# Kernel tuning notes

Measured on AMD Instinct MI355X. Metric: run time of the kernel, lower is better.

The kernel has to match this reference:

```python
import jax, jax.numpy as jnp
import numpy as np

N_NODES = 100000
N_EDGES = 1600000
NIN = 128
NHID = 128
N_GRAPHS = 1024


def _gcn_conv(x, src, dst, norm, W, b, n_nodes):
    """PyG-style GCNConv: linear (no bias) -> normalized scatter-add -> + bias."""
    xw = x @ W                                   # [N, out]
    msg = xw[src] * norm[:, None]                # gather + edge-normalize, [E', out]
    out = jax.ops.segment_sum(msg, dst, num_segments=n_nodes)
    return out + b


def _gcn_norm(edge_index, n_nodes):
    """Add self-loops and compute symmetric deg^{-1/2} normalization per edge."""
    loops = jnp.arange(n_nodes, dtype=edge_index.dtype)
    src = jnp.concatenate([edge_index[0], loops])
    dst = jnp.concatenate([edge_index[1], loops])
    deg = jax.ops.segment_sum(jnp.ones_like(dst, dtype=jnp.float32), dst,
                              num_segments=n_nodes)
    deg_isqrt = jnp.where(deg > 0, jax.lax.rsqrt(jnp.maximum(deg, 1.0)), 0.0)
    norm = deg_isqrt[src] * deg_isqrt[dst]
    return src, dst, norm


def setup_inputs() -> dict:
    key = jax.random.key(0)
    ks = jax.random.split(key, 8)
    x = jax.random.normal(ks[0], (N_NODES, NIN), dtype=jnp.float32)
    edge_index = jax.random.randint(ks[1], (2, N_EDGES), 0, N_NODES, dtype=jnp.int64)
    batch = jnp.sort(jax.random.randint(ks[2], (N_NODES,), 0, N_GRAPHS, dtype=jnp.int64))
    s_in = 1.0 / np.sqrt(NIN)
    s_h = 1.0 / np.sqrt(NHID)
    return {
        "x": x,
        "edge_index": edge_index,
        "batch": batch,
        "W1": jax.random.normal(ks[3], (NIN, NHID), dtype=jnp.float32) * s_in,
        "b1": jnp.zeros((NHID,), dtype=jnp.float32),
        "W2": jax.random.normal(ks[4], (NHID, NHID), dtype=jnp.float32) * s_h,
        "b2": jnp.zeros((NHID,), dtype=jnp.float32),
        "W3": jax.random.normal(ks[5], (NHID, NHID), dtype=jnp.float32) * s_h,
        "b3": jnp.zeros((NHID,), dtype=jnp.float32),
        "Wfc": jax.random.normal(ks[6], (NHID, 1), dtype=jnp.float32) * s_h,
        "bfc": jnp.zeros((1,), dtype=jnp.float32),
    }


def reference(x, edge_index, batch, W1, b1, W2, b2, W3, b3, Wfc, bfc):
    n_nodes = x.shape[0]
    src, dst, norm = _gcn_norm(edge_index, n_nodes)
    h = jax.nn.relu(_gcn_conv(x, src, dst, norm, W1, b1, n_nodes))
    h = jax.nn.relu(_gcn_conv(h, src, dst, norm, W2, b2, n_nodes))
    h = jax.nn.relu(_gcn_conv(h, src, dst, norm, W3, b3, n_nodes))
    # global mean pool over graphs in the batch
    sums = jax.ops.segment_sum(h, batch, num_segments=N_GRAPHS)      # [G, NHID]
    cnts = jax.ops.segment_sum(jnp.ones((n_nodes,), dtype=h.dtype), batch,
                               num_segments=N_GRAPHS)
    pooled = sums / jnp.maximum(cnts, 1.0)[:, None]
    return pooled @ Wfc + bfc                                        # [G, 1]
```

## Files before the change

### kernel.cpp

```cpp
#include <hip/hip_runtime.h>

#define N_NODES   100000
#define N_EDGES   1600000
#define NFEAT     128
#define N_GRAPHS  1024

#define BSHIFT  8
#define BNODES  256
#define NBUCK   391
#define BCAP    4608
#define SC_EDGES 8192
#define SC_BLOCKS 196

typedef unsigned int uint32;
typedef unsigned short ushort;
typedef __attribute__((ext_vector_type(8))) short short8;
typedef __attribute__((ext_vector_type(4))) float f32x4;

__device__ inline ushort f2b(float f) {
    uint32 x = __float_as_uint(f);
    uint32 r = x + 0x7fffu + ((x >> 16) & 1u);
    return (ushort)(r >> 16);
}
__device__ inline float blo(uint32 u) { return __uint_as_float(u << 16); }
__device__ inline float bhi(uint32 u) { return __uint_as_float(u & 0xffff0000u); }

__global__ __launch_bounds__(256) void k_scatter(const int* __restrict__ src, const int* __restrict__ dst,
                                                 int* __restrict__ cur, uint32* __restrict__ bbuf) {
    __shared__ int hist[NBUCK];
    __shared__ int lofs[NBUCK];
    __shared__ int lcur[NBUCK];
    __shared__ int gbase[NBUCK];
    __shared__ int wsum[4];
    __shared__ uint32 sortedP[SC_EDGES];
    __shared__ ushort sortedB[SC_EDGES];
    int t = threadIdx.x;
    int e0 = blockIdx.x * SC_EDGES;
    int total = N_EDGES - e0; if (total > SC_EDGES) total = SC_EDGES; if (total < 0) total = 0;

    for (int i = t; i < NBUCK; i += 256) hist[i] = 0;
    __syncthreads();
    for (int i = t; i < total; i += 256)
        atomicAdd(&hist[dst[e0 + i] >> BSHIFT], 1);
    __syncthreads();
    {
        int b0 = 2 * t, b1 = 2 * t + 1;
        int h0 = (b0 < NBUCK) ? hist[b0] : 0;
        int h1 = (b1 < NBUCK) ? hist[b1] : 0;
        int ts = h0 + h1;
        int lane = t & 63, w = t >> 6;
        int inc = ts;
        #pragma unroll
        for (int d = 1; d < 64; d <<= 1) {
            int u = __shfl_up(inc, d, 64);
            if (lane >= d) inc += u;
        }
        if (lane == 63) wsum[w] = inc;
        __syncthreads();
        int wpre = 0;
        for (int i = 0; i < w; ++i) wpre += wsum[i];
        int run = wpre + inc - ts;
        if (b0 < NBUCK) {
            lofs[b0] = run; lcur[b0] = run;
            if (h0) gbase[b0] = atomicAdd(&cur[b0], h0);
        }
        if (b1 < NBUCK) {
            lofs[b1] = run + h0; lcur[b1] = run + h0;
            if (h1) gbase[b1] = atomicAdd(&cur[b1], h1);
        }
    }
    __syncthreads();
    for (int i = t; i < total; i += 256) {
        int s = src[e0 + i], d = dst[e0 + i];
        int b = d >> BSHIFT;
        int p = atomicAdd(&lcur[b], 1);
        sortedP[p] = ((uint32)(d & (BNODES - 1)) << 17) | (uint32)s;
        sortedB[p] = (ushort)b;
    }
    __syncthreads();
    for (int i = t; i < total; i += 256) {
        int b = sortedB[i];
        int addr = gbase[b] + (i - lofs[b]);
        if (addr < BCAP)
            bbuf[(size_t)b * BCAP + addr] = sortedP[i];
    }
}

__global__ __launch_bounds__(256) void k_bucketscan(const int* __restrict__ cur, int* __restrict__ bucketBase,
                                                    int* __restrict__ offsets) {
    __shared__ int wsum[4];
    int t = threadIdx.x;
    int b0 = 2 * t, b1 = 2 * t + 1;
    int h0 = 0, h1 = 0;
    if (b0 < NBUCK) { h0 = cur[b0]; if (h0 > BCAP) h0 = BCAP; }
    if (b1 < NBUCK) { h1 = cur[b1]; if (h1 > BCAP) h1 = BCAP; }
    int ts = h0 + h1;
    int lane = t & 63, w = t >> 6;
    int inc = ts;
    #pragma unroll
    for (int d = 1; d < 64; d <<= 1) {
        int u = __shfl_up(inc, d, 64);
        if (lane >= d) inc += u;
    }
    if (lane == 63) wsum[w] = inc;
    __syncthreads();
    int wpre = 0;
    for (int i = 0; i < w; ++i) wpre += wsum[i];
    int run = wpre + inc - ts;
    if (b0 < NBUCK) bucketBase[b0] = run;
    if (b1 < NBUCK) bucketBase[b1] = run + h0;
    if (t == 255) offsets[N_NODES] = run + ts;
}

__global__ __launch_bounds__(256) void k_build(const uint32* __restrict__ bbuf, const int* __restrict__ cur,
                                               const int* __restrict__ bucketBase, int* __restrict__ col,
                                               int* __restrict__ offsets, float* __restrict__ dinv) {
    int b = blockIdx.x;
    __shared__ int hist[BNODES], lcur[BNODES];
    __shared__ int wsum[4];
    __shared__ int sorted[BCAP];
    int t = threadIdx.x;
    int cnt = cur[b]; if (cnt > BCAP) cnt = BCAP;
    const uint32* reg = bbuf + (size_t)b * BCAP;
    hist[t] = 0;
    __syncthreads();
    for (int i = t; i < cnt; i += 256) atomicAdd(&hist[reg[i] >> 17], 1);
    __syncthreads();
    {
        int c = hist[t];
        int lane = t & 63, w = t >> 6;
        int inc = c;
        #pragma unroll
        for (int d = 1; d < 64; d <<= 1) {
            int u = __shfl_up(inc, d, 64);
            if (lane >= d) inc += u;
        }
        if (lane == 63) wsum[w] = inc;
        __syncthreads();
        int wpre = 0;
        for (int i = 0; i < w; ++i) wpre += wsum[i];
        int excl = wpre + inc - c;
        lcur[t] = excl;
        int node = (b << BSHIFT) + t;
        if (node < N_NODES) {
            offsets[node] = bucketBase[b] + excl;
            dinv[node] = rsqrtf((float)(c + 1));
        }
    }
    __syncthreads();
    for (int i = t; i < cnt; i += 256) {
        uint32 p = reg[i];
        int lp = atomicAdd(&lcur[p >> 17], 1);
        sorted[lp] = (int)(p & 0x1FFFF);
    }
    __syncthreads();
    int base = bucketBase[b];
    for (int i = t; i < cnt; i += 256) col[base + i] = sorted[i];
}

__global__ __launch_bounds__(256) void k_castw(const float* __restrict__ W1, const float* __restrict__ W2,
                                               const float* __restrict__ W3, ushort* __restrict__ WT) {
    int i = blockIdx.x * blockDim.x + threadIdx.x;
    if (i >= 3 * NFEAT * NFEAT) return;
    int l = i >> 14;
    int j = i & 16383;
    int n = j >> 7;
    int k = j & 127;
    const float* W = (l == 0) ? W1 : (l == 1) ? W2 : W3;
    WT[i] = f2b(W[k * NFEAT + n]);
}

#define WT_STRIDE 136
#define GEMM_EPILOGUE \
    __syncthreads(); \
    { \
        ushort* sC = sWT; \
        int colBase = lane & 15; \
        _Pragma("unroll") \
        for (int r = 0; r < 4; ++r) { \
            int lr = wave * 16 + kg * 4 + r; \
            _Pragma("unroll") \
            for (int nt = 0; nt < 8; ++nt) \
                sC[lr * NFEAT + nt * 16 + colBase] = f2b(acc[nt][r]); \
        } \
    } \
    __syncthreads(); \
    { \
        int rowBase = blockIdx.x * 128; \
        const float4* sC4 = (const float4*)sWT; \
        for (int i = t; i < 2048; i += 512) { \
            int row = i >> 4; \
            int gr = rowBase + row; \
            if (gr < M) ((float4*)(C + (size_t)gr * NFEAT))[i & 15] = sC4[i]; \
        } \
    }

__global__ __launch_bounds__(512) void k_gemm(const ushort* __restrict__ A,
                                              const ushort* __restrict__ WTl,
                                              ushort* __restrict__ C, int M) {
    __shared__ ushort sWT[NFEAT * WT_STRIDE];
    int t = threadIdx.x;
    for (int i = t; i < NFEAT * 16; i += 512) {
        int n = i >> 4, c = i & 15;
        *(float4*)(sWT + n * WT_STRIDE + c * 8) = ((const float4*)WTl)[i];
    }
    int wave = t >> 6, lane = t & 63;
    int m0 = blockIdx.x * 128 + wave * 16;
    int mRow = m0 + (lane & 15);
    if (mRow >= M) mRow = M - 1;
    int kg = lane >> 4;
    const short8* Ap = (const short8*)(A + (size_t)mRow * NFEAT + kg * 8);
    short8 a0 = Ap[0];
    short8 a1 = Ap[4];
    short8 a2 = Ap[8];
    short8 a3 = Ap[12];
    __syncthreads();

    f32x4 acc[8];
    #pragma unroll
    for (int nt = 0; nt < 8; ++nt) acc[nt] = (f32x4){0.f, 0.f, 0.f, 0.f};

    #pragma unroll
    for (int nt = 0; nt < 8; ++nt) {
        int n = nt * 16 + (lane & 15);
        const short8* Bp = (const short8*)(sWT + n * WT_STRIDE + kg * 8);
        short8 b0 = Bp[0];
        short8 b1 = Bp[4];
        short8 b2 = Bp[8];
        short8 b3 = Bp[12];
        acc[nt] = __builtin_amdgcn_mfma_f32_16x16x32_bf16(a0, b0, acc[nt], 0, 0, 0);
        acc[nt] = __builtin_amdgcn_mfma_f32_16x16x32_bf16(a1, b1, acc[nt], 0, 0, 0);
        acc[nt] = __builtin_amdgcn_mfma_f32_16x16x32_bf16(a2, b2, acc[nt], 0, 0, 0);
        acc[nt] = __builtin_amdgcn_mfma_f32_16x16x32_bf16(a3, b3, acc[nt], 0, 0, 0);
    }
    GEMM_EPILOGUE
}

__device__ inline short8 cvt8(const float* p) {
    float4 v0 = ((const float4*)p)[0];
    float4 v1 = ((const float4*)p)[1];
    short8 r;
    r[0] = (short)f2b(v0.x); r[1] = (short)f2b(v0.y);
    r[2] = (short)f2b(v0.z); r[3] = (short)f2b(v0.w);
    r[4] = (short)f2b(v1.x); r[5] = (short)f2b(v1.y);
    r[6] = (short)f2b(v1.z); r[7] = (short)f2b(v1.w);
    return r;
}

__global__ __launch_bounds__(512) void k_gemm_x(const float* __restrict__ A,
                                                const ushort* __restrict__ WTl,
                                                ushort* __restrict__ C, int M) {
    __shared__ ushort sWT[NFEAT * WT_STRIDE];
    int t = threadIdx.x;
    for (int i = t; i < NFEAT * 16; i += 512) {
        int n = i >> 4, c = i & 15;
        *(float4*)(sWT + n * WT_STRIDE + c * 8) = ((const float4*)WTl)[i];
    }
    int wave = t >> 6, lane = t & 63;
    int m0 = blockIdx.x * 128 + wave * 16;
    int mRow = m0 + (lane & 15);
    if (mRow >= M) mRow = M - 1;
    int kg = lane >> 4;
    const float* Ap = A + (size_t)mRow * NFEAT + kg * 8;
    short8 a0 = cvt8(Ap);
    short8 a1 = cvt8(Ap + 32);
    short8 a2 = cvt8(Ap + 64);
    short8 a3 = cvt8(Ap + 96);
    __syncthreads();

    f32x4 acc[8];
    #pragma unroll
    for (int nt = 0; nt < 8; ++nt) acc[nt] = (f32x4){0.f, 0.f, 0.f, 0.f};

    #pragma unroll
    for (int nt = 0; nt < 8; ++nt) {
        int n = nt * 16 + (lane & 15);
        const short8* Bp = (const short8*)(sWT + n * WT_STRIDE + kg * 8);
        short8 b0 = Bp[0];
        short8 b1 = Bp[4];
        short8 b2 = Bp[8];
        short8 b3 = Bp[12];
        acc[nt] = __builtin_amdgcn_mfma_f32_16x16x32_bf16(a0, b0, acc[nt], 0, 0, 0);
        acc[nt] = __builtin_amdgcn_mfma_f32_16x16x32_bf16(a1, b1, acc[nt], 0, 0, 0);
        acc[nt] = __builtin_amdgcn_mfma_f32_16x16x32_bf16(a2, b2, acc[nt], 0, 0, 0);
        acc[nt] = __builtin_amdgcn_mfma_f32_16x16x32_bf16(a3, b3, acc[nt], 0, 0, 0);
    }
    GEMM_EPILOGUE
}

#define AGG_BODY4 \
    float dn = dinv[n]; \
    int half = lane >> 4; \
    int fl = lane & 15; \
    const uint4* XW4 = (const uint4*)XWu; \
    uint4 sv = XW4[(size_t)n * 16 + fl]; \
    float ws = (half == 0) ? dn * dn : 0.f; \
    float a0 = ws * blo(sv.x), a1 = ws * bhi(sv.x); \
    float a2 = ws * blo(sv.y), a3 = ws * bhi(sv.y); \
    float a4 = ws * blo(sv.z), a5 = ws * bhi(sv.z); \
    float a6 = ws * blo(sv.w), a7 = ws * bhi(sv.w); \
    int e0 = off[n], e1 = off[n + 1]; \
    for (int base = e0; base < e1; base += 64) { \
        int len = e1 - base; if (len > 64) len = 64; \
        int cm = (lane < len) ? col[base + lane] : 0; \
        float wm = (lane < len) ? dn * dinv[cm] : 0.f; \
        int j = 0; \
        for (; j + 16 <= len; j += 16) { \
            uint4 u[4]; float w[4]; \
            _Pragma("unroll") \
            for (int p = 0; p < 4; ++p) { \
                int idx = j + 4 * p + half; \
                int cc = __shfl(cm, idx, 64); \
                w[p] = __shfl(wm, idx, 64); \
                u[p] = XW4[(size_t)cc * 16 + fl]; \
            } \
            _Pragma("unroll") \
            for (int p = 0; p < 4; ++p) { \
                a0 = fmaf(w[p], blo(u[p].x), a0); a1 = fmaf(w[p], bhi(u[p].x), a1); \
                a2 = fmaf(w[p], blo(u[p].y), a2); a3 = fmaf(w[p], bhi(u[p].y), a3); \
                a4 = fmaf(w[p], blo(u[p].z), a4); a5 = fmaf(w[p], bhi(u[p].z), a5); \
                a6 = fmaf(w[p], blo(u[p].w), a6); a7 = fmaf(w[p], bhi(u[p].w), a7); \
            } \
        } \
        for (; j < len; j += 4) { \
            int rem = len - j; \
            int idx = j + ((half < rem) ? half : 0); \
            int cc = __shfl(cm, idx, 64); \
            float ww = __shfl(wm, idx, 64); \
            if (half >= rem) ww = 0.f; \
            uint4 u = XW4[(size_t)cc * 16 + fl]; \
            a0 = fmaf(ww, blo(u.x), a0); a1 = fmaf(ww, bhi(u.x), a1); \
            a2 = fmaf(ww, blo(u.y), a2); a3 = fmaf(ww, bhi(u.y), a3); \
            a4 = fmaf(ww, blo(u.z), a4); a5 = fmaf(ww, bhi(u.z), a5); \
            a6 = fmaf(ww, blo(u.w), a6); a7 = fmaf(ww, bhi(u.w), a7); \
        } \
    } \
    a0 += __shfl_xor(a0, 32, 64); a0 += __shfl_xor(a0, 16, 64); \
    a1 += __shfl_xor(a1, 32, 64); a1 += __shfl_xor(a1, 16, 64); \
    a2 += __shfl_xor(a2, 32, 64); a2 += __shfl_xor(a2, 16, 64); \
    a3 += __shfl_xor(a3, 32, 64); a3 += __shfl_xor(a3, 16, 64); \
    a4 += __shfl_xor(a4, 32, 64); a4 += __shfl_xor(a4, 16, 64); \
    a5 += __shfl_xor(a5, 32, 64); a5 += __shfl_xor(a5, 16, 64); \
    a6 += __shfl_xor(a6, 32, 64); a6 += __shfl_xor(a6, 16, 64); \
    a7 += __shfl_xor(a7, 32, 64); a7 += __shfl_xor(a7, 16, 64);

__global__ __launch_bounds__(256) void k_agg(const uint32* __restrict__ XWu, const int* __restrict__ col,
                                             const int* __restrict__ off, const float* __restrict__ dinv,
                                             const float* __restrict__ bias, uint32* __restrict__ Hu) {
    int wid = (blockIdx.x * blockDim.x + threadIdx.x) >> 6;
    int lane = threadIdx.x & 63;
    if (wid >= N_NODES) return;
    int n = wid;
    AGG_BODY4
    if (half == 0) {
        float4 bb0 = ((const float4*)bias)[2 * fl];
        float4 bb1 = ((const float4*)bias)[2 * fl + 1];
        float r0 = fmaxf(a0 + bb0.x, 0.f), r1 = fmaxf(a1 + bb0.y, 0.f);
        float r2 = fmaxf(a2 + bb0.z, 0.f), r3 = fmaxf(a3 + bb0.w, 0.f);
        float r4 = fmaxf(a4 + bb1.x, 0.f), r5 = fmaxf(a5 + bb1.y, 0.f);
        float r6 = fmaxf(a6 + bb1.z, 0.f), r7 = fmaxf(a7 + bb1.w, 0.f);
        uint4 o;
        o.x = (uint32)f2b(r0) | ((uint32)f2b(r1) << 16);
        o.y = (uint32)f2b(r2) | ((uint32)f2b(r3) << 16);
        o.z = (uint32)f2b(r4) | ((uint32)f2b(r5) << 16);
        o.w = (uint32)f2b(r6) | ((uint32)f2b(r7) << 16);
        ((uint4*)Hu)[(size_t)n * 16 + fl] = o;
    }
}

__global__ __launch_bounds__(256) void k_agg_fc(const uint32* __restrict__ XWu, const int* __restrict__ col,
                                                const int* __restrict__ off, const float* __restrict__ dinv,
                                                const float* __restrict__ bias, const float* __restrict__ Wfc,
                                                float* __restrict__ nodeS) {
    int wid = (blockIdx.x * blockDim.x + threadIdx.x) >> 6;
    int lane = threadIdx.x & 63;
    if (wid >= N_NODES) return;
    int n = wid;
    AGG_BODY4
    float4 bb0 = ((const float4*)bias)[2 * fl];
    float4 bb1 = ((const float4*)bias)[2 * fl + 1];
    float4 wf0 = ((const float4*)Wfc)[2 * fl];
    float4 wf1 = ((const float4*)Wfc)[2 * fl + 1];
    float s = fmaxf(a0 + bb0.x, 0.f) * wf0.x + fmaxf(a1 + bb0.y, 0.f) * wf0.y
            + fmaxf(a2 + bb0.z, 0.f) * wf0.z + fmaxf(a3 + bb0.w, 0.f) * wf0.w
            + fmaxf(a4 + bb1.x, 0.f) * wf1.x + fmaxf(a5 + bb1.y, 0.f) * wf1.y
            + fmaxf(a6 + bb1.z, 0.f) * wf1.z + fmaxf(a7 + bb1.w, 0.f) * wf1.w;
    s += __shfl_xor(s, 8, 64);
    s += __shfl_xor(s, 4, 64);
    s += __shfl_xor(s, 2, 64);
    s += __shfl_xor(s, 1, 64);
    if (lane == 0) nodeS[n] = s;
}

__device__ inline int lower_bound_dev(const int* a, int n, int key) {
    int lo = 0, hi = n;
    while (lo < hi) {
        int mid = (lo + hi) >> 1;
        if (a[mid] < key) lo = mid + 1; else hi = mid;
    }
    return lo;
}

__global__ __launch_bounds__(256) void k_pool(const float* __restrict__ nodeS, const int* __restrict__ batch,
                                              const float* __restrict__ bfc, float* __restrict__ out) {
    int g = blockIdx.x;
    int t = threadIdx.x;
    int lo = lower_bound_dev(batch, N_NODES, g);
    int hi = lower_bound_dev(batch, N_NODES, g + 1);
    float s = 0.f;
    for (int i = lo + t; i < hi; i += 256) s += nodeS[i];
    for (int d = 32; d > 0; d >>= 1) s += __shfl_down(s, d, 64);
    __shared__ float ws[4];
    int lane = t & 63, w = t >> 6;
    if (lane == 0) ws[w] = s;
    __syncthreads();
    if (t == 0) {
        float tot = ws[0] + ws[1] + ws[2] + ws[3];
        float cnt = (float)(hi - lo);
        out[g] = tot / fmaxf(cnt, 1.0f) + bfc[0];
    }
}

extern "C" void kernel_launch(void* const* d_in, const int* in_sizes, int n_in,
                              void* d_out, int out_size, void* d_ws, size_t ws_size,
                              hipStream_t stream) {
    const float* x    = (const float*)d_in[0];
    const int*   ei   = (const int*)d_in[1];
    const int*   batch= (const int*)d_in[2];
    const float* W1   = (const float*)d_in[3];
    const float* b1   = (const float*)d_in[4];
    const float* W2   = (const float*)d_in[5];
    const float* b2   = (const float*)d_in[6];
    const float* W3   = (const float*)d_in[7];
    const float* b3   = (const float*)d_in[8];
    const float* Wfc  = (const float*)d_in[9];
    const float* bfc  = (const float*)d_in[10];
    float* out = (float*)d_out;

    const int* src = ei;
    const int* dst = ei + N_EDGES;

    char* p = (char*)d_ws;
    auto carve = [&](size_t bytes) { void* r = (void*)p; p += (bytes + 255) & ~(size_t)255; return r; };
    int*    cur       = (int*)   carve(sizeof(int) * NBUCK);
    uint32* bbuf      = (uint32*)carve(sizeof(uint32) * (size_t)NBUCK * BCAP);
    int*    bucketBase= (int*)   carve(sizeof(int) * (NBUCK + 1));
    float*  dinv      = (float*) carve(sizeof(float) * N_NODES);
    int*    offsets   = (int*)   carve(sizeof(int) * (N_NODES + 1));
    int*    col       = (int*)   carve(sizeof(int) * N_EDGES);
    ushort* XW        = (ushort*)carve(sizeof(short) * (size_t)N_NODES * NFEAT);
    ushort* H         = (ushort*)carve(sizeof(short) * (size_t)N_NODES * NFEAT);
    ushort* WT        = (ushort*)carve(sizeof(short) * 3 * NFEAT * NFEAT);
    float*  nodeS     = (float*) carve(sizeof(float) * N_NODES);

    const int waveNodeBlocks = (N_NODES * 64 + 255) / 256;
    const int gemmBlocks = (N_NODES + 127) / 128;

    hipMemsetAsync(cur, 0, sizeof(int) * NBUCK, stream);
    k_scatter<<<SC_BLOCKS, 256, 0, stream>>>(src, dst, cur, bbuf);
    k_bucketscan<<<1, 256, 0, stream>>>(cur, bucketBase, offsets);
    k_build<<<NBUCK, 256, 0, stream>>>(bbuf, cur, bucketBase, col, offsets, dinv);

    k_castw<<<(3 * NFEAT * NFEAT + 255) / 256, 256, 0, stream>>>(W1, W2, W3, WT);

    k_gemm_x<<<gemmBlocks, 512, 0, stream>>>(x, WT, XW, N_NODES);
    k_agg<<<waveNodeBlocks, 256, 0, stream>>>((const uint32*)XW, col, offsets, dinv, b1, (uint32*)H);
    k_gemm<<<gemmBlocks, 512, 0, stream>>>(H, WT + NFEAT * NFEAT, XW, N_NODES);
    k_agg<<<waveNodeBlocks, 256, 0, stream>>>((const uint32*)XW, col, offsets, dinv, b2, (uint32*)H);
    k_gemm<<<gemmBlocks, 512, 0, stream>>>(H, WT + 2 * NFEAT * NFEAT, XW, N_NODES);
    k_agg_fc<<<waveNodeBlocks, 256, 0, stream>>>((const uint32*)XW, col, offsets, dinv, b3, Wfc, nodeS);

    k_pool<<<N_GRAPHS, 256, 0, stream>>>(nodeS, batch, bfc, out);
}
```

Measured before the change: 392.4 us.

## Fold bucket scan into build and weight cast into GEMMs; persistent multi-tile GEMM

Removes the standalone single-block bucket-scan kernel: each build block now computes its own bucket base by reducing the clamped bucket counts, and the last block writes the total edge count. Removes the weight-cast kernel: each GEMM block converts and transposes the fp32 weights into bf16 shared memory itself. The GEMM is restructured so each block keeps its B fragments in registers and loops over four 64-row tiles, with waves split across column halves. This cuts two launches and their serial dependencies, at the cost of redundant weight conversion and bucket reduction per block and more register pressure.

New measurement: 419.0 us. 1.07x slower.

```diff
diff --git a/kernel.cpp b/kernel.cpp
--- a/kernel.cpp
+++ b/kernel.cpp
@@ -86,44 +86,42 @@
     }
 }
 
-__global__ __launch_bounds__(256) void k_bucketscan(const int* __restrict__ cur, int* __restrict__ bucketBase,
-                                                    int* __restrict__ offsets) {
-    __shared__ int wsum[4];
-    int t = threadIdx.x;
-    int b0 = 2 * t, b1 = 2 * t + 1;
-    int h0 = 0, h1 = 0;
-    if (b0 < NBUCK) { h0 = cur[b0]; if (h0 > BCAP) h0 = BCAP; }
-    if (b1 < NBUCK) { h1 = cur[b1]; if (h1 > BCAP) h1 = BCAP; }
-    int ts = h0 + h1;
-    int lane = t & 63, w = t >> 6;
-    int inc = ts;
-    #pragma unroll
-    for (int d = 1; d < 64; d <<= 1) {
-        int u = __shfl_up(inc, d, 64);
-        if (lane >= d) inc += u;
-    }
-    if (lane == 63) wsum[w] = inc;
-    __syncthreads();
-    int wpre = 0;
-    for (int i = 0; i < w; ++i) wpre += wsum[i];
-    int run = wpre + inc - ts;
-    if (b0 < NBUCK) bucketBase[b0] = run;
-    if (b1 < NBUCK) bucketBase[b1] = run + h0;
-    if (t == 255) offsets[N_NODES] = run + ts;
-}
-
 __global__ __launch_bounds__(256) void k_build(const uint32* __restrict__ bbuf, const int* __restrict__ cur,
-                                               const int* __restrict__ bucketBase, int* __restrict__ col,
-                                               int* __restrict__ offsets, float* __restrict__ dinv) {
+                                               int* __restrict__ col, int* __restrict__ offsets,
+                                               float* __restrict__ dinv) {
     int b = blockIdx.x;
     __shared__ int hist[BNODES], lcur[BNODES];
-    __shared__ int wsum[4];
+    __shared__ int wsum[4], wtot[4];
     __shared__ int sorted[BCAP];
+    __shared__ int sBase, sTotal;
     int t = threadIdx.x;
+    {
+        int pre = 0, tot = 0;
+        #pragma unroll
+        for (int q = 0; q < 2; ++q) {
+            int i = 2 * t + q;
+            if (i < NBUCK) {
+                int v = cur[i]; if (v > BCAP) v = BCAP;
+                tot += v;
+                if (i < b) pre += v;
+            }
+        }
+        int lane = t & 63, w = t >> 6;
+        #pragma unroll
+        for (int d = 32; d > 0; d >>= 1) { pre += __shfl_down(pre, d, 64); tot += __shfl_down(tot, d, 64); }
+        if (lane == 0) { wsum[w] = pre; wtot[w] = tot; }
+        __syncthreads();
+        if (t == 0) {
+            sBase = wsum[0] + wsum[1] + wsum[2] + wsum[3];
+            sTotal = wtot[0] + wtot[1] + wtot[2] + wtot[3];
+        }
+        hist[t] = 0;
+    }
+    __syncthreads();
+    int base = sBase;
+    if (b == NBUCK - 1 && t == 0) offsets[N_NODES] = sTotal;
     int cnt = cur[b]; if (cnt > BCAP) cnt = BCAP;
     const uint32* reg = bbuf + (size_t)b * BCAP;
-    hist[t] = 0;
-    __syncthreads();
     for (int i = t; i < cnt; i += 256) atomicAdd(&hist[reg[i] >> 17], 1);
     __syncthreads();
     {
@@ -143,7 +141,7 @@
         lcur[t] = excl;
         int node = (b << BSHIFT) + t;
         if (node < N_NODES) {
-            offsets[node] = bucketBase[b] + excl;
+            offsets[node] = base + excl;
             dinv[node] = rsqrtf((float)(c + 1));
         }
     }
@@ -154,86 +152,81 @@
         sorted[lp] = (int)(p & 0x1FFFF);
     }
     __syncthreads();
-    int base = bucketBase[b];
     for (int i = t; i < cnt; i += 256) col[base + i] = sorted[i];
 }
 
-__global__ __launch_bounds__(256) void k_castw(const float* __restrict__ W1, const float* __restrict__ W2,
-                                               const float* __restrict__ W3, ushort* __restrict__ WT) {
-    int i = blockIdx.x * blockDim.x + threadIdx.x;
-    if (i >= 3 * NFEAT * NFEAT) return;
-    int l = i >> 14;
-    int j = i & 16383;
-    int n = j >> 7;
-    int k = j & 127;
-    const float* W = (l == 0) ? W1 : (l == 1) ? W2 : W3;
-    WT[i] = f2b(W[k * NFEAT + n]);
-}
-
 #define WT_STRIDE 136
-#define GEMM_EPILOGUE \
+#define GEMM_TILES 4
+
+#define GEMM_PROLOGUE(AFRAG_LOADS) \
+    __shared__ ushort sWT[NFEAT * WT_STRIDE];    \
+    __shared__ ushort sC[64 * NFEAT];            \
+    int t = threadIdx.x; \
+     \
+    for (int i = t; i < NFEAT * 32; i += 512) { \
+        int k = i >> 5, n0 = (i & 31) * 4; \
+        float4 v = ((const float4*)Wl)[i]; \
+        sWT[(n0 + 0) * WT_STRIDE + k] = f2b(v.x); \
+        sWT[(n0 + 1) * WT_STRIDE + k] = f2b(v.y); \
+        sWT[(n0 + 2) * WT_STRIDE + k] = f2b(v.z); \
+        sWT[(n0 + 3) * WT_STRIDE + k] = f2b(v.w); \
+    } \
+    int wave = t >> 6, lane = t & 63; \
+    int ch = wave & 1;           \
+    int rg = wave >> 1;          \
+    int kg = lane >> 4; \
+    int colBase = lane & 15; \
     __syncthreads(); \
-    { \
-        ushort* sC = sWT; \
-        int colBase = lane & 15; \
+     \
+    short8 bfr[4][4]; \
+    _Pragma("unroll") \
+    for (int nt = 0; nt < 4; ++nt) { \
+        int n = ch * 64 + nt * 16 + colBase; \
+        const short8* Bp = (const short8*)(sWT + n * WT_STRIDE + kg * 8); \
+        bfr[nt][0] = Bp[0]; bfr[nt][1] = Bp[4]; bfr[nt][2] = Bp[8]; bfr[nt][3] = Bp[12]; \
+    } \
+    int blockBase = blockIdx.x * (64 * GEMM_TILES); \
+    for (int tile = 0; tile < GEMM_TILES; ++tile) { \
+        int tb = blockBase + tile * 64; \
+        int m0 = tb + rg * 16; \
+        int mRow = m0 + colBase; \
+        if (mRow >= M) mRow = M - 1; \
+        short8 a0, a1, a2, a3; \
+        AFRAG_LOADS \
+        f32x4 acc[4]; \
+        _Pragma("unroll") \
+        for (int nt = 0; nt < 4; ++nt) acc[nt] = (f32x4){0.f, 0.f, 0.f, 0.f}; \
+        _Pragma("unroll") \
+        for (int nt = 0; nt < 4; ++nt) { \
+            acc[nt] = __builtin_amdgcn_mfma_f32_16x16x32_bf16(a0, bfr[nt][0], acc[nt], 0, 0, 0); \
+            acc[nt] = __builtin_amdgcn_mfma_f32_16x16x32_bf16(a1, bfr[nt][1], acc[nt], 0, 0, 0); \
+            acc[nt] = __builtin_amdgcn_mfma_f32_16x16x32_bf16(a2, bfr[nt][2], acc[nt], 0, 0, 0); \
+            acc[nt] = __builtin_amdgcn_mfma_f32_16x16x32_bf16(a3, bfr[nt][3], acc[nt], 0, 0, 0); \
+        } \
+        __syncthreads();    \
         _Pragma("unroll") \
         for (int r = 0; r < 4; ++r) { \
-            int lr = wave * 16 + kg * 4 + r; \
+            int rowLocal = rg * 16 + kg * 4 + r; \
             _Pragma("unroll") \
-            for (int nt = 0; nt < 8; ++nt) \
-                sC[lr * NFEAT + nt * 16 + colBase] = f2b(acc[nt][r]); \
+            for (int nt = 0; nt < 4; ++nt) \
+                sC[rowLocal * NFEAT + ch * 64 + nt * 16 + colBase] = f2b(acc[nt][r]); \
         } \
-    } \
-    __syncthreads(); \
-    { \
-        int rowBase = blockIdx.x * 128; \
-        const float4* sC4 = (const float4*)sWT; \
-        for (int i = t; i < 2048; i += 512) { \
+        __syncthreads(); \
+        const float4* sC4 = (const float4*)sC; \
+        for (int i = t; i < 1024; i += 512) { \
             int row = i >> 4; \
-            int gr = rowBase + row; \
+            int gr = tb + row; \
             if (gr < M) ((float4*)(C + (size_t)gr * NFEAT))[i & 15] = sC4[i]; \
         } \
     }
 
 __global__ __launch_bounds__(512) void k_gemm(const ushort* __restrict__ A,
-                                              const ushort* __restrict__ WTl,
+                                              const float* __restrict__ Wl,
                                               ushort* __restrict__ C, int M) {
-    __shared__ ushort sWT[NFEAT * WT_STRIDE];
-    int t = threadIdx.x;
-    for (int i = t; i < NFEAT * 16; i += 512) {
-        int n = i >> 4, c = i & 15;
-        *(float4*)(sWT + n * WT_STRIDE + c * 8) = ((const float4*)WTl)[i];
-    }
-    int wave = t >> 6, lane = t & 63;
-    int m0 = blockIdx.x * 128 + wave * 16;
-    int mRow = m0 + (lane & 15);
-    if (mRow >= M) mRow = M - 1;
-    int kg = lane >> 4;
-    const short8* Ap = (const short8*)(A + (size_t)mRow * NFEAT + kg * 8);
-    short8 a0 = Ap[0];
-    short8 a1 = Ap[4];
-    short8 a2 = Ap[8];
-    short8 a3 = Ap[12];
-    __syncthreads();
-
-    f32x4 acc[8];
-    #pragma unroll
-    for (int nt = 0; nt < 8; ++nt) acc[nt] = (f32x4){0.f, 0.f, 0.f, 0.f};
-
-    #pragma unroll
-    for (int nt = 0; nt < 8; ++nt) {
-        int n = nt * 16 + (lane & 15);
-        const short8* Bp = (const short8*)(sWT + n * WT_STRIDE + kg * 8);
-        short8 b0 = Bp[0];
-        short8 b1 = Bp[4];
-        short8 b2 = Bp[8];
-        short8 b3 = Bp[12];
-        acc[nt] = __builtin_amdgcn_mfma_f32_16x16x32_bf16(a0, b0, acc[nt], 0, 0, 0);
-        acc[nt] = __builtin_amdgcn_mfma_f32_16x16x32_bf16(a1, b1, acc[nt], 0, 0, 0);
-        acc[nt] = __builtin_amdgcn_mfma_f32_16x16x32_bf16(a2, b2, acc[nt], 0, 0, 0);
-        acc[nt] = __builtin_amdgcn_mfma_f32_16x16x32_bf16(a3, b3, acc[nt], 0, 0, 0);
-    }
-    GEMM_EPILOGUE
+    GEMM_PROLOGUE({
+        const short8* Ap = (const short8*)(A + (size_t)mRow * NFEAT + kg * 8);
+        a0 = Ap[0]; a1 = Ap[4]; a2 = Ap[8]; a3 = Ap[12];
+    })
 }
 
 __device__ inline short8 cvt8(const float* p) {
@@ -248,44 +241,12 @@
 }
 
 __global__ __launch_bounds__(512) void k_gemm_x(const float* __restrict__ A,
-                                                const ushort* __restrict__ WTl,
+                                                const float* __restrict__ Wl,
                                                 ushort* __restrict__ C, int M) {
-    __shared__ ushort sWT[NFEAT * WT_STRIDE];
-    int t = threadIdx.x;
-    for (int i = t; i < NFEAT * 16; i += 512) {
-        int n = i >> 4, c = i & 15;
-        *(float4*)(sWT + n * WT_STRIDE + c * 8) = ((const float4*)WTl)[i];
-    }
-    int wave = t >> 6, lane = t & 63;
-    int m0 = blockIdx.x * 128 + wave * 16;
-    int mRow = m0 + (lane & 15);
-    if (mRow >= M) mRow = M - 1;
-    int kg = lane >> 4;
-    const float* Ap = A + (size_t)mRow * NFEAT + kg * 8;
-    short8 a0 = cvt8(Ap);
-    short8 a1 = cvt8(Ap + 32);
-    short8 a2 = cvt8(Ap + 64);
-    short8 a3 = cvt8(Ap + 96);
-    __syncthreads();
-
-    f32x4 acc[8];
-    #pragma unroll
-    for (int nt = 0; nt < 8; ++nt) acc[nt] = (f32x4){0.f, 0.f, 0.f, 0.f};
-
-    #pragma unroll
-    for (int nt = 0; nt < 8; ++nt) {
-        int n = nt * 16 + (lane & 15);
-        const short8* Bp = (const short8*)(sWT + n * WT_STRIDE + kg * 8);
-        short8 b0 = Bp[0];
-        short8 b1 = Bp[4];
-        short8 b2 = Bp[8];
-        short8 b3 = Bp[12];
-        acc[nt] = __builtin_amdgcn_mfma_f32_16x16x32_bf16(a0, b0, acc[nt], 0, 0, 0);
-        acc[nt] = __builtin_amdgcn_mfma_f32_16x16x32_bf16(a1, b1, acc[nt], 0, 0, 0);
-        acc[nt] = __builtin_amdgcn_mfma_f32_16x16x32_bf16(a2, b2, acc[nt], 0, 0, 0);
-        acc[nt] = __builtin_amdgcn_mfma_f32_16x16x32_bf16(a3, b3, acc[nt], 0, 0, 0);
-    }
-    GEMM_EPILOGUE
+    GEMM_PROLOGUE({
+        const float* Ap = A + (size_t)mRow * NFEAT + kg * 8;
+        a0 = cvt8(Ap); a1 = cvt8(Ap + 32); a2 = cvt8(Ap + 64); a3 = cvt8(Ap + 96);
+    })
 }
 
 #define AGG_BODY4 \
@@ -444,30 +405,25 @@
     auto carve = [&](size_t bytes) { void* r = (void*)p; p += (bytes + 255) & ~(size_t)255; return r; };
     int*    cur       = (int*)   carve(sizeof(int) * NBUCK);
     uint32* bbuf      = (uint32*)carve(sizeof(uint32) * (size_t)NBUCK * BCAP);
-    int*    bucketBase= (int*)   carve(sizeof(int) * (NBUCK + 1));
     float*  dinv      = (float*) carve(sizeof(float) * N_NODES);
     int*    offsets   = (int*)   carve(sizeof(int) * (N_NODES + 1));
     int*    col       = (int*)   carve(sizeof(int) * N_EDGES);
     ushort* XW        = (ushort*)carve(sizeof(short) * (size_t)N_NODES * NFEAT);
     ushort* H         = (ushort*)carve(sizeof(short) * (size_t)N_NODES * NFEAT);
-    ushort* WT        = (ushort*)carve(sizeof(short) * 3 * NFEAT * NFEAT);
     float*  nodeS     = (float*) carve(sizeof(float) * N_NODES);
 
     const int waveNodeBlocks = (N_NODES * 64 + 255) / 256;
-    const int gemmBlocks = (N_NODES + 127) / 128;
+    const int gemmBlocks = (N_NODES + 64 * GEMM_TILES - 1) / (64 * GEMM_TILES);
 
     hipMemsetAsync(cur, 0, sizeof(int) * NBUCK, stream);
     k_scatter<<<SC_BLOCKS, 256, 0, stream>>>(src, dst, cur, bbuf);
-    k_bucketscan<<<1, 256, 0, stream>>>(cur, bucketBase, offsets);
-    k_build<<<NBUCK, 256, 0, stream>>>(bbuf, cur, bucketBase, col, offsets, dinv);
-
-    k_castw<<<(3 * NFEAT * NFEAT + 255) / 256, 256, 0, stream>>>(W1, W2, W3, WT);
-
-    k_gemm_x<<<gemmBlocks, 512, 0, stream>>>(x, WT, XW, N_NODES);
+    k_build<<<NBUCK, 256, 0, stream>>>(bbuf, cur, col, offsets, dinv);
+
+    k_gemm_x<<<gemmBlocks, 512, 0, stream>>>(x, W1, XW, N_NODES);
     k_agg<<<waveNodeBlocks, 256, 0, stream>>>((const uint32*)XW, col, offsets, dinv, b1, (uint32*)H);
-    k_gemm<<<gemmBlocks, 512, 0, stream>>>(H, WT + NFEAT * NFEAT, XW, N_NODES);
+    k_gemm<<<gemmBlocks, 512, 0, stream>>>(H, W2, XW, N_NODES);
     k_agg<<<waveNodeBlocks, 256, 0, stream>>>((const uint32*)XW, col, offsets, dinv, b2, (uint32*)H);
-    k_gemm<<<gemmBlocks, 512, 0, stream>>>(H, WT + 2 * NFEAT * NFEAT, XW, N_NODES);
+    k_gemm<<<gemmBlocks, 512, 0, stream>>>(H, W3, XW, N_NODES);
     k_agg_fc<<<waveNodeBlocks, 256, 0, stream>>>((const uint32*)XW, col, offsets, dinv, b3, Wfc, nodeS);
 
     k_pool<<<N_GRAPHS, 256, 0, stream>>>(nodeS, batch, bfc, out);
```

## Register-cache edges in scatter/build and fold bucket scan into build

Applied to the files above, without the earlier changes.

The scatter and build kernels now read each edge once into registers. They record a per-bucket or per-node ticket from the histogram atomic, then place edges using prefix offsets plus the ticket. This removes the second global read and the second pass of shared-memory atomics. The separate single-block bucket-scan kernel is removed, and each build block computes its own base by reducing the bucket counts below it. This saves one launch and one serialization point in exchange for higher register pressure and redundant per-block reductions.

New measurement: 383.5 us. 1.02x faster.

```diff
diff --git a/kernel.cpp b/kernel.cpp
--- a/kernel.cpp
+++ b/kernel.cpp
@@ -10,7 +10,9 @@
 #define NBUCK   391
 #define BCAP    4608
 #define SC_EDGES 8192
+#define SC_EPT   32
 #define SC_BLOCKS 196
+#define BD_EPT   18
 
 typedef unsigned int uint32;
 typedef unsigned short ushort;
@@ -29,7 +31,6 @@
                                                  int* __restrict__ cur, uint32* __restrict__ bbuf) {
     __shared__ int hist[NBUCK];
     __shared__ int lofs[NBUCK];
-    __shared__ int lcur[NBUCK];
     __shared__ int gbase[NBUCK];
     __shared__ int wsum[4];
     __shared__ uint32 sortedP[SC_EDGES];
@@ -40,8 +41,21 @@
 
     for (int i = t; i < NBUCK; i += 256) hist[i] = 0;
     __syncthreads();
-    for (int i = t; i < total; i += 256)
-        atomicAdd(&hist[dst[e0 + i] >> BSHIFT], 1);
+
+    uint32 val[SC_EPT];
+    int    meta[SC_EPT];
+    #pragma unroll
+    for (int k = 0; k < SC_EPT; ++k) {
+        int i = t + k * 256;
+        meta[k] = -1;
+        if (i < total) {
+            int s = src[e0 + i], d = dst[e0 + i];
+            int b = d >> BSHIFT;
+            int tk = atomicAdd(&hist[b], 1);
+            val[k] = ((uint32)(d & (BNODES - 1)) << 17) | (uint32)s;
+            meta[k] = (b << 13) | tk;
+        }
+    }
     __syncthreads();
     {
         int b0 = 2 * t, b1 = 2 * t + 1;
@@ -61,21 +75,23 @@
         for (int i = 0; i < w; ++i) wpre += wsum[i];
         int run = wpre + inc - ts;
         if (b0 < NBUCK) {
-            lofs[b0] = run; lcur[b0] = run;
+            lofs[b0] = run;
             if (h0) gbase[b0] = atomicAdd(&cur[b0], h0);
         }
         if (b1 < NBUCK) {
-            lofs[b1] = run + h0; lcur[b1] = run + h0;
+            lofs[b1] = run + h0;
             if (h1) gbase[b1] = atomicAdd(&cur[b1], h1);
         }
     }
     __syncthreads();
-    for (int i = t; i < total; i += 256) {
-        int s = src[e0 + i], d = dst[e0 + i];
-        int b = d >> BSHIFT;
-        int p = atomicAdd(&lcur[b], 1);
-        sortedP[p] = ((uint32)(d & (BNODES - 1)) << 17) | (uint32)s;
-        sortedB[p] = (ushort)b;
+    #pragma unroll
+    for (int k = 0; k < SC_EPT; ++k) {
+        if (meta[k] >= 0) {
+            int b = meta[k] >> 13;
+            int p = lofs[b] + (meta[k] & 0x1FFF);
+            sortedP[p] = val[k];
+            sortedB[p] = (ushort)b;
+        }
     }
     __syncthreads();
     for (int i = t; i < total; i += 256) {
@@ -86,45 +102,57 @@
     }
 }
 
-__global__ __launch_bounds__(256) void k_bucketscan(const int* __restrict__ cur, int* __restrict__ bucketBase,
-                                                    int* __restrict__ offsets) {
-    __shared__ int wsum[4];
+__global__ __launch_bounds__(256) void k_build(const uint32* __restrict__ bbuf, const int* __restrict__ cur,
+                                               int* __restrict__ col, int* __restrict__ offsets,
+                                               float* __restrict__ dinv) {
+    int b = blockIdx.x;
+    __shared__ int hist[BNODES], excl[BNODES];
+    __shared__ int wsum[4], wtot[4];
+    __shared__ int sorted[BCAP];
+    __shared__ int sBase, sTotal;
     int t = threadIdx.x;
-    int b0 = 2 * t, b1 = 2 * t + 1;
-    int h0 = 0, h1 = 0;
-    if (b0 < NBUCK) { h0 = cur[b0]; if (h0 > BCAP) h0 = BCAP; }
-    if (b1 < NBUCK) { h1 = cur[b1]; if (h1 > BCAP) h1 = BCAP; }
-    int ts = h0 + h1;
-    int lane = t & 63, w = t >> 6;
-    int inc = ts;
-    #pragma unroll
-    for (int d = 1; d < 64; d <<= 1) {
-        int u = __shfl_up(inc, d, 64);
-        if (lane >= d) inc += u;
-    }
-    if (lane == 63) wsum[w] = inc;
-    __syncthreads();
-    int wpre = 0;
-    for (int i = 0; i < w; ++i) wpre += wsum[i];
-    int run = wpre + inc - ts;
-    if (b0 < NBUCK) bucketBase[b0] = run;
-    if (b1 < NBUCK) bucketBase[b1] = run + h0;
-    if (t == 255) offsets[N_NODES] = run + ts;
-}
-
-__global__ __launch_bounds__(256) void k_build(const uint32* __restrict__ bbuf, const int* __restrict__ cur,
-                                               const int* __restrict__ bucketBase, int* __restrict__ col,
-                                               int* __restrict__ offsets, float* __restrict__ dinv) {
-    int b = blockIdx.x;
-    __shared__ int hist[BNODES], lcur[BNODES];
-    __shared__ int wsum[4];
-    __shared__ int sorted[BCAP];
-    int t = threadIdx.x;
+    {
+        int pre = 0, tot = 0;
+        #pragma unroll
+        for (int q = 0; q < 2; ++q) {
+            int i = 2 * t + q;
+            if (i < NBUCK) {
+                int v = cur[i]; if (v > BCAP) v = BCAP;
+                tot += v;
+                if (i < b) pre += v;
+            }
+        }
+        int lane = t & 63, w = t >> 6;
+        #pragma unroll
+        for (int d = 32; d > 0; d >>= 1) { pre += __shfl_down(pre, d, 64); tot += __shfl_down(tot, d, 64); }
+        if (lane == 0) { wsum[w] = pre; wtot[w] = tot; }
+        __syncthreads();
+        if (t == 0) {
+            sBase = wsum[0] + wsum[1] + wsum[2] + wsum[3];
+            sTotal = wtot[0] + wtot[1] + wtot[2] + wtot[3];
+        }
+        hist[t] = 0;
+    }
+    __syncthreads();
+    int base = sBase;
+    if (b == NBUCK - 1 && t == 0) offsets[N_NODES] = sTotal;
     int cnt = cur[b]; if (cnt > BCAP) cnt = BCAP;
     const uint32* reg = bbuf + (size_t)b * BCAP;
-    hist[t] = 0;
-    __syncthreads();
-    for (int i = t; i < cnt; i += 256) atomicAdd(&hist[reg[i] >> 17], 1);
+
+    uint32 val[BD_EPT];
+    int    meta[BD_EPT];
+    #pragma unroll
+    for (int k = 0; k < BD_EPT; ++k) {
+        int i = t + k * 256;
+        meta[k] = -1;
+        if (i < cnt) {
+            uint32 p = reg[i];
+            int node = p >> 17;
+            int tk = atomicAdd(&hist[node], 1);
+            val[k] = p & 0x1FFFF;
+            meta[k] = (node << 16) | tk;
+        }
+    }
     __syncthreads();
     {
         int c = hist[t];
@@ -139,22 +167,23 @@
         __syncthreads();
         int wpre = 0;
         for (int i = 0; i < w; ++i) wpre += wsum[i];
-        int excl = wpre + inc - c;
-        lcur[t] = excl;
+        int e = wpre + inc - c;
+        excl[t] = e;
         int node = (b << BSHIFT) + t;
         if (node < N_NODES) {
-            offsets[node] = bucketBase[b] + excl;
+            offsets[node] = base + e;
             dinv[node] = rsqrtf((float)(c + 1));
         }
     }
     __syncthreads();
-    for (int i = t; i < cnt; i += 256) {
-        uint32 p = reg[i];
-        int lp = atomicAdd(&lcur[p >> 17], 1);
-        sorted[lp] = (int)(p & 0x1FFFF);
-    }
-    __syncthreads();
-    int base = bucketBase[b];
+    #pragma unroll
+    for (int k = 0; k < BD_EPT; ++k) {
+        if (meta[k] >= 0) {
+            int node = meta[k] >> 16;
+            sorted[excl[node] + (meta[k] & 0xFFFF)] = (int)val[k];
+        }
+    }
+    __syncthreads();
     for (int i = t; i < cnt; i += 256) col[base + i] = sorted[i];
 }
 
@@ -444,7 +473,6 @@
     auto carve = [&](size_t bytes) { void* r = (void*)p; p += (bytes + 255) & ~(size_t)255; return r; };
     int*    cur       = (int*)   carve(sizeof(int) * NBUCK);
     uint32* bbuf      = (uint32*)carve(sizeof(uint32) * (size_t)NBUCK * BCAP);
-    int*    bucketBase= (int*)   carve(sizeof(int) * (NBUCK + 1));
     float*  dinv      = (float*) carve(sizeof(float) * N_NODES);
     int*    offsets   = (int*)   carve(sizeof(int) * (N_NODES + 1));
     int*    col       = (int*)   carve(sizeof(int) * N_EDGES);
@@ -458,8 +486,7 @@
 
     hipMemsetAsync(cur, 0, sizeof(int) * NBUCK, stream);
     k_scatter<<<SC_BLOCKS, 256, 0, stream>>>(src, dst, cur, bbuf);
-    k_bucketscan<<<1, 256, 0, stream>>>(cur, bucketBase, offsets);
-    k_build<<<NBUCK, 256, 0, stream>>>(bbuf, cur, bucketBase, col, offsets, dinv);
+    k_build<<<NBUCK, 256, 0, stream>>>(bbuf, cur, col, offsets, dinv);
 
     k_castw<<<(3 * NFEAT * NFEAT + 255) / 256, 256, 0, stream>>>(W1, W2, W3, WT);
 
```
